# Kernel optimization log

Hardware: AMD Instinct MI355X
Metric: run time of the kernel (lower is better)

## Reference

```python
import jax, jax.numpy as jnp
import numpy as np

B, S, D = 1, 4096, 768
H = 12
HD = D // H  # 64


def setup_inputs() -> dict:
    key = jax.random.key(0)
    ks = jax.random.split(key, 6)
    sc = 1.0 / np.sqrt(D)
    return {
        "x": jax.random.normal(ks[0], (B, S, D), dtype=jnp.float32),
        "wq": jax.random.normal(ks[1], (D, D), dtype=jnp.float32) * sc,
        "wk": jax.random.normal(ks[2], (D, D), dtype=jnp.float32) * sc,
        "wv": jax.random.normal(ks[3], (D, D), dtype=jnp.float32) * sc,
        "wo": jax.random.normal(ks[4], (D, D), dtype=jnp.float32) * sc,
        "bo": jax.random.normal(ks[5], (D,), dtype=jnp.float32) * 0.02,
    }


def reference(x, wq, wk, wv, wo, bo):
    b, n, _ = x.shape
    # projections (torch Linear: x @ W.T; here weights stored as (d_in, d_out))
    q = (x @ wq).reshape(b, n, H, HD).transpose(0, 2, 1, 3)  # b h n d
    k = (x @ wk).reshape(b, n, H, HD).transpose(0, 2, 1, 3)
    v = (x @ wv).reshape(b, n, H, HD).transpose(0, 2, 1, 3)
    scores = jnp.einsum("bhqd,bhkd->bhqk", q, k)
    causal = jnp.tril(jnp.ones((n, n), dtype=bool))  # True = keep
    scores = jnp.where(causal, scores, -jnp.inf)
    weights = jax.nn.softmax(scores / np.sqrt(HD), axis=-1)
    ctx = jnp.einsum("bhqk,bhkd->bhqd", weights, v)
    ctx = ctx.transpose(0, 2, 1, 3).reshape(b, n, D)
    return ctx @ wo + bo
```

## Files before the change

kernel.cpp:

```cpp
#include <hip/hip_runtime.h>


typedef short bf16x8 __attribute__((ext_vector_type(8)));
typedef float f32x4 __attribute__((ext_vector_type(4)));
typedef unsigned short u16;

static constexpr int S_LEN = 4096;
static constexpr int DIM   = 768;
static constexpr int NH    = 12;
static constexpr float QSCALE = 0.125f * 1.44269504088896340736f;

__device__ inline u16 f2bf(float f) {
  union { float f; unsigned int u; } v; v.f = f;
  unsigned int r = v.u + 0x7FFFu + ((v.u >> 16) & 1u);
  return (u16)(r >> 16);
}

__device__ inline void gload_lds16(const u16* g, u16* s) {
  __builtin_amdgcn_global_load_lds(
      (const __attribute__((address_space(1))) unsigned int*)g,
      (__attribute__((address_space(3))) unsigned int*)s, 16, 0, 0);
}

__global__ __launch_bounds__(256)
void prep_kernel(const float* __restrict__ x, const float* __restrict__ w0,
                 const float* __restrict__ w1, const float* __restrict__ w2,
                 const float* __restrict__ w3, u16* __restrict__ xb,
                 u16* __restrict__ t0, u16* __restrict__ t1,
                 u16* __restrict__ t2, u16* __restrict__ t3) {
  if (blockIdx.z == 4) {
    const size_t n = (size_t)S_LEN * DIM;
    const int id = blockIdx.y * 12 + blockIdx.x;
    const size_t stride = (size_t)144 * 256 * 8;
    for (size_t i = ((size_t)id * 256 + threadIdx.x) * 8; i < n; i += stride) {
      const float4 a = *(const float4*)(x + i);
      const float4 b = *(const float4*)(x + i + 4);
      bf16x8 o;
      o[0] = (short)f2bf(a.x); o[1] = (short)f2bf(a.y);
      o[2] = (short)f2bf(a.z); o[3] = (short)f2bf(a.w);
      o[4] = (short)f2bf(b.x); o[5] = (short)f2bf(b.y);
      o[6] = (short)f2bf(b.z); o[7] = (short)f2bf(b.w);
      *(bf16x8*)(xb + i) = o;
    }
    return;
  }
  __shared__ float T[64][65];
  const float* src; u16* dst;
  switch (blockIdx.z) {
    case 0: src = w0; dst = t0; break;
    case 1: src = w1; dst = t1; break;
    case 2: src = w2; dst = t2; break;
    default: src = w3; dst = t3; break;
  }
  const int k0 = blockIdx.y * 64, n0 = blockIdx.x * 64;
  const int r = threadIdx.x >> 2, c0 = (threadIdx.x & 3) * 16;
#pragma unroll
  for (int i = 0; i < 4; ++i) {
    const float4 v = *(const float4*)(src + (size_t)(k0 + r) * DIM + n0 + c0 + i * 4);
    T[r][c0 + i * 4 + 0] = v.x;
    T[r][c0 + i * 4 + 1] = v.y;
    T[r][c0 + i * 4 + 2] = v.z;
    T[r][c0 + i * 4 + 3] = v.w;
  }
  __syncthreads();
  bf16x8 o0, o1;
#pragma unroll
  for (int i = 0; i < 8; ++i) {
    o0[i] = (short)f2bf(T[c0 + i][r]);
    o1[i] = (short)f2bf(T[c0 + 8 + i][r]);
  }
  *(bf16x8*)(dst + (size_t)(n0 + r) * DIM + k0 + c0) = o0;
  *(bf16x8*)(dst + (size_t)(n0 + r) * DIM + k0 + c0 + 8) = o1;
}

template <int MODE>
__global__ __launch_bounds__(256)
void mfma_gemm_kernel(const u16* __restrict__ A, const u16* __restrict__ Bq,
                      const u16* __restrict__ Bk, const u16* __restrict__ Bv,
                      const float* __restrict__ bias, u16* __restrict__ Qb,
                      u16* __restrict__ Kb, u16* __restrict__ VT,
                      float* __restrict__ Out) {
  constexpr int MT = (MODE == 0) ? 4 : 2;
  constexpr int BM = MT * 32;
  __shared__ __align__(16) u16 Al[BM * 64];
  __shared__ __align__(16) u16 Bl[96 * 64];

  const int tid  = threadIdx.x;
  const int wv   = tid >> 6;
  const int lane = tid & 63;
  const int quad = lane >> 4;
  const int l16  = lane & 15;
  const int wr = wv >> 1, wc = wv & 1;
  const int m0 = blockIdx.y * BM;
  const int n0 = blockIdx.x * 96;

  int wi = 0, nb = n0;
  const u16* BT = Bq;
  if (MODE == 0) {
    wi = n0 / DIM;
    nb = n0 - wi * DIM;
    BT = (wi == 0) ? Bq : (wi == 1) ? Bk : Bv;
  }

  const int sr8 = lane >> 3;
  const int sc  = ((lane & 7) ^ sr8) * 8;
  const int key = (l16 & 7);

  f32x4 acc[MT][3] = {};

  for (int k0 = 0; k0 < DIM; k0 += 64) {
    __syncthreads();
#pragma unroll
    for (int j = 0; j < MT; ++j)
      gload_lds16(A + (size_t)(m0 + wv * (BM / 4) + j * 8 + sr8) * DIM + k0 + sc,
                  &Al[(wv * (BM / 4) + j * 8) * 64]);
#pragma unroll
    for (int j = 0; j < 3; ++j)
      gload_lds16(BT + (size_t)(nb + wv * 24 + j * 8 + sr8) * DIM + k0 + sc,
                  &Bl[(wv * 24 + j * 8) * 64]);
    __syncthreads();

#pragma unroll
    for (int kh = 0; kh < 2; ++kh) {
      const int cb = kh * 4;
      bf16x8 af[MT], bfr[3];
#pragma unroll
      for (int mt = 0; mt < MT; ++mt) {
        const int row = wr * (BM / 2) + mt * 16 + l16;
        af[mt] = *(const bf16x8*)&Al[row * 64 + ((cb + quad) ^ key) * 8];
      }
#pragma unroll
      for (int nt = 0; nt < 3; ++nt) {
        const int row = wc * 48 + nt * 16 + l16;
        bfr[nt] = *(const bf16x8*)&Bl[row * 64 + ((cb + quad) ^ key) * 8];
      }
#pragma unroll
      for (int mt = 0; mt < MT; ++mt)
#pragma unroll
        for (int nt = 0; nt < 3; ++nt)
          acc[mt][nt] = __builtin_amdgcn_mfma_f32_16x16x32_bf16(
              af[mt], bfr[nt], acc[mt][nt], 0, 0, 0);
    }
  }

  const float sc_out = (MODE == 0 && wi == 0) ? QSCALE : 1.0f;
#pragma unroll
  for (int mt = 0; mt < MT; ++mt) {
#pragma unroll
    for (int nt = 0; nt < 3; ++nt) {
      const int row = m0 + wr * (BM / 2) + mt * 16 + quad * 4;
      const int nc  = wc * 48 + nt * 16 + l16;
      if (MODE == 0) {
        const int ncol = nb + nc;
        if (wi < 2) {
          u16* dst = (wi == 0) ? Qb : Kb;
#pragma unroll
          for (int r = 0; r < 4; ++r)
            dst[(size_t)(row + r) * DIM + ncol] = f2bf(acc[mt][nt][r] * sc_out);
        } else {
          u16 pk[4];
#pragma unroll
          for (int r = 0; r < 4; ++r) pk[r] = f2bf(acc[mt][nt][r]);
          unsigned long long v;
          __builtin_memcpy(&v, pk, 8);
          *(unsigned long long*)(VT + (size_t)ncol * S_LEN + row) = v;
        }
      } else {
        const int ncol = n0 + nc;
        const float bvv = bias[ncol];
#pragma unroll
        for (int r = 0; r < 4; ++r)
          Out[(size_t)(row + r) * DIM + ncol] = acc[mt][nt][r] + bvv;
      }
    }
  }
}

__global__ __launch_bounds__(256)
void attn_mfma_kernel(const u16* __restrict__ Qb, const u16* __restrict__ Kb,
                      const u16* __restrict__ VTb, u16* __restrict__ ctx) {
  __shared__ __align__(16) u16 Ql[32 * 72];
  __shared__ __align__(16) u16 Kl[128 * 64];
  __shared__ __align__(16) u16 Vl[64 * 128];
  __shared__ __align__(16) u16 Pl[4][16 * 72];
  __shared__ float4 lbuf[4][64];

  const int tid  = threadIdx.x;
  const int w    = tid >> 6;
  const int lane = tid & 63;
  const int quad = lane >> 4;
  const int l16  = lane & 15;
  const int qw   = w >> 1;
  const int kw   = w & 1;
  const int key  = l16 & 7;

  const int id = blockIdx.x;
  const int rc = id & 7, slot = id >> 3;
  const int h  = (slot < 64) ? rc : 8 + (rc >> 1);
  const int bx = (slot < 64) ? slot : ((rc & 1) * 32 + (slot - 64));

  const int sr8  = lane >> 3;
  const int scK  = ((lane & 7) ^ sr8) * 8;
  const int sr16 = lane >> 4;

#pragma unroll 1
  for (int side = 0; side < 2; ++side) {
    const int qt = side ? (127 - bx) : bx;
    const int q0 = qt * 32;

    __syncthreads();
    {
      const int row = tid >> 3, col = (tid & 7) * 8;
      *(bf16x8*)&Ql[row * 72 + col] =
          *(const bf16x8*)(Qb + (size_t)(q0 + row) * DIM + h * 64 + col);
    }

    f32x4 o[4] = {};
    float l_r[4] = {};

    const int nkt = qt / 2 + 1;
    const int niter = (nkt + 1) >> 1;
    const int my_last = nkt - 1;

#pragma unroll 1
    for (int i = 0; i < niter; ++i) {
      const int k0g = i * 128;
      __syncthreads();
#pragma unroll
      for (int j = 0; j < 4; ++j)
        gload_lds16(Kb + (size_t)(k0g + w * 32 + j * 8 + sr8) * DIM + h * 64 + scK,
                    &Kl[(w * 32 + j * 8) * 64]);
#pragma unroll
      for (int j = 0; j < 4; ++j) {
        const int vrow = w * 16 + j * 4 + sr16;
        const int vcol = ((lane & 15) ^ (vrow & 7)) * 8;
        gload_lds16(VTb + (size_t)(h * 64 + vrow) * S_LEN + k0g + vcol,
                    &Vl[(w * 16 + j * 4) * 128]);
      }
      __syncthreads();

      const int kt_w = 2 * i + kw;
      if (kt_w < nkt) {
        const bf16x8 aq0 = *(const bf16x8*)&Ql[(qw * 16 + l16) * 72 + quad * 8];
        const bf16x8 aq1 = *(const bf16x8*)&Ql[(qw * 16 + l16) * 72 + 32 + quad * 8];
        f32x4 s[4];
#pragma unroll
        for (int t = 0; t < 4; ++t) {
          const int row = kw * 64 + t * 16 + l16;
          const bf16x8 bk0 = *(const bf16x8*)&Kl[row * 64 + (quad ^ key) * 8];
          const bf16x8 bk1 = *(const bf16x8*)&Kl[row * 64 + ((quad ^ 4) ^ key) * 8];
          s[t] = __builtin_amdgcn_mfma_f32_16x16x32_bf16(aq0, bk0, f32x4{0.f,0.f,0.f,0.f}, 0, 0, 0);
          s[t] = __builtin_amdgcn_mfma_f32_16x16x32_bf16(aq1, bk1, s[t], 0, 0, 0);
        }

        if (kt_w == my_last) {
#pragma unroll
          for (int t = 0; t < 4; ++t)
#pragma unroll
            for (int r = 0; r < 4; ++r) {
              const int kvg = k0g + kw * 64 + t * 16 + l16;
              const int qg  = q0 + qw * 16 + quad * 4 + r;
              float p = __builtin_amdgcn_exp2f(s[t][r]);
              if (kvg > qg) p = 0.f;
              l_r[r] += p;
              Pl[w][(quad * 4 + r) * 72 + t * 16 + l16] =
                  (u16)((__float_as_uint(p) + 0x8000u) >> 16);
            }
        } else {
#pragma unroll
          for (int t = 0; t < 4; ++t)
#pragma unroll
            for (int r = 0; r < 4; ++r) {
              const float p = __builtin_amdgcn_exp2f(s[t][r]);
              l_r[r] += p;
              Pl[w][(quad * 4 + r) * 72 + t * 16 + l16] =
                  (u16)((__float_as_uint(p) + 0x8000u) >> 16);
            }
        }

        const bf16x8 pa0 = *(const bf16x8*)&Pl[w][l16 * 72 + quad * 8];
        const bf16x8 pa1 = *(const bf16x8*)&Pl[w][l16 * 72 + 32 + quad * 8];
#pragma unroll
        for (int t = 0; t < 4; ++t) {
          const int row = t * 16 + l16;
          const int c0 = (kw * 8 + quad) ^ key;
          const int c1 = (kw * 8 + quad + 4) ^ key;
          const bf16x8 vb0 = *(const bf16x8*)&Vl[row * 128 + c0 * 8];
          const bf16x8 vb1 = *(const bf16x8*)&Vl[row * 128 + c1 * 8];
          o[t] = __builtin_amdgcn_mfma_f32_16x16x32_bf16(pa0, vb0, o[t], 0, 0, 0);
          o[t] = __builtin_amdgcn_mfma_f32_16x16x32_bf16(pa1, vb1, o[t], 0, 0, 0);
        }
      }
    }

    __syncthreads();
    float* Obuf = (float*)Kl;
#pragma unroll
    for (int t = 0; t < 4; ++t)
      *(f32x4*)&Obuf[(w * 64 + lane) * 16 + t * 4] = o[t];
    lbuf[w][lane] = float4{l_r[0], l_r[1], l_r[2], l_r[3]};
    __syncthreads();
#pragma unroll
    for (int t = 0; t < 4; ++t) {
      const f32x4 po = *(const f32x4*)&Obuf[((w ^ 1) * 64 + lane) * 16 + t * 4];
      o[t] += po;
    }
    {
      const float4 pl = lbuf[w ^ 1][lane];
      l_r[0] += pl.x; l_r[1] += pl.y; l_r[2] += pl.z; l_r[3] += pl.w;
    }

    if (kw == 0) {
#pragma unroll
      for (int r = 0; r < 4; ++r) {
        float l = l_r[r];
        l += __shfl_xor(l, 1);
        l += __shfl_xor(l, 2);
        l += __shfl_xor(l, 4);
        l += __shfl_xor(l, 8);
        const float inv = 1.f / l;
        const int row = q0 + qw * 16 + quad * 4 + r;
#pragma unroll
        for (int t = 0; t < 4; ++t)
          ctx[(size_t)row * DIM + h * 64 + t * 16 + l16] = f2bf(o[t][r] * inv);
      }
    }
  }
}

extern "C" void kernel_launch(void* const* d_in, const int* in_sizes, int n_in,
                              void* d_out, int out_size, void* d_ws,
                              size_t ws_size, hipStream_t stream) {
  const float* x  = (const float*)d_in[0];
  const float* wq = (const float*)d_in[1];
  const float* wk = (const float*)d_in[2];
  const float* wv = (const float*)d_in[3];
  const float* wo = (const float*)d_in[4];
  const float* bo = (const float*)d_in[5];

  const size_t n_x = (size_t)S_LEN * DIM;
  const size_t n_w = (size_t)DIM * DIM;
  u16* xb  = (u16*)d_ws;
  u16* wtq = xb + n_x;
  u16* wtk = wtq + n_w;
  u16* wtv = wtk + n_w;
  u16* wto = wtv + n_w;
  u16* Qb  = wto + n_w;
  u16* Kb  = Qb + n_x;
  u16* VTb = Kb + n_x;
  u16* ctx = VTb + n_x;

  prep_kernel<<<dim3(12, 12, 5), 256, 0, stream>>>(
      x, wq, wk, wv, wo, xb, wtq, wtk, wtv, wto);

  mfma_gemm_kernel<0><<<dim3(24, 32), 256, 0, stream>>>(
      xb, wtq, wtk, wtv, nullptr, Qb, Kb, VTb, nullptr);

  attn_mfma_kernel<<<dim3(768), 256, 0, stream>>>(Qb, Kb, VTb, ctx);

  mfma_gemm_kernel<1><<<dim3(8, 64), 256, 0, stream>>>(
      ctx, wto, nullptr, nullptr, bo, nullptr, nullptr, nullptr, (float*)d_out);
}
```

Baseline: 183.0 us.

## Process both causal query tiles in one KV pass with double-buffered K/V

The attention kernel now loads both paired query tiles (front and mirrored back) at once, with each of four waves owning 16 query rows, and streams 64-key K/V tiles through a double-buffered LDS ring. The next tile is prefetched while the current one is computed. This drops the split-K-across-waves reduction through LDS and the second pass over K/V for the low tile, which lets the two tiles share K/V loads. In exchange, waves on the short tile go idle for much of the loop, so load balance across waves is worse, and there is only one barrier per iteration with async loads in flight.

```diff
diff --git a/kernel.cpp b/kernel.cpp
--- a/kernel.cpp
+++ b/kernel.cpp
@@ -179,19 +179,16 @@
 __global__ __launch_bounds__(256)
 void attn_mfma_kernel(const u16* __restrict__ Qb, const u16* __restrict__ Kb,
                       const u16* __restrict__ VTb, u16* __restrict__ ctx) {
-  __shared__ __align__(16) u16 Ql[32 * 72];
-  __shared__ __align__(16) u16 Kl[128 * 64];
-  __shared__ __align__(16) u16 Vl[64 * 128];
+  __shared__ __align__(16) u16 Ql[64 * 72];
+  __shared__ __align__(16) u16 Kl[2][64 * 64];
+  __shared__ __align__(16) u16 Vl[2][64 * 64];
   __shared__ __align__(16) u16 Pl[4][16 * 72];
-  __shared__ float4 lbuf[4][64];
 
   const int tid  = threadIdx.x;
   const int w    = tid >> 6;
   const int lane = tid & 63;
   const int quad = lane >> 4;
   const int l16  = lane & 15;
-  const int qw   = w >> 1;
-  const int kw   = w & 1;
   const int key  = l16 & 7;
 
   const int id = blockIdx.x;
@@ -199,132 +196,117 @@
   const int h  = (slot < 64) ? rc : 8 + (rc >> 1);
   const int bx = (slot < 64) ? slot : ((rc & 1) * 32 + (slot - 64));
 
-  const int sr8  = lane >> 3;
-  const int scK  = ((lane & 7) ^ sr8) * 8;
-  const int sr16 = lane >> 4;
+  const int q0A = bx * 32;
+  const int q0B = (127 - bx) * 32;
+  const int qlo = ((w < 2) ? q0A : q0B) + (w & 1) * 16;
+  const int nkt_w = ((qlo + 15) >> 6) + 1;
+  const int nktB  = ((q0B + 31) >> 6) + 1;
+
+  const int sr8 = lane >> 3;
+  const int sc  = ((lane & 7) ^ sr8) * 8;
+
+  {
+    const int qrow_s = tid >> 3;
+    const int qcol_s = (tid & 7) * 8;
+    *(bf16x8*)&Ql[qrow_s * 72 + qcol_s] =
+        *(const bf16x8*)(Qb + (size_t)(q0A + qrow_s) * DIM + h * 64 + qcol_s);
+    *(bf16x8*)&Ql[(32 + qrow_s) * 72 + qcol_s] =
+        *(const bf16x8*)(Qb + (size_t)(q0B + qrow_s) * DIM + h * 64 + qcol_s);
+  }
+#pragma unroll
+  for (int j = 0; j < 2; ++j) {
+    gload_lds16(Kb + (size_t)(w * 16 + j * 8 + sr8) * DIM + h * 64 + sc,
+                &Kl[0][(w * 16 + j * 8) * 64]);
+    gload_lds16(VTb + (size_t)(h * 64 + w * 16 + j * 8 + sr8) * S_LEN + sc,
+                &Vl[0][(w * 16 + j * 8) * 64]);
+  }
+  __syncthreads();
+
+  const bf16x8 aq0 = *(const bf16x8*)&Ql[(w * 16 + l16) * 72 + quad * 8];
+  const bf16x8 aq1 = *(const bf16x8*)&Ql[(w * 16 + l16) * 72 + 32 + quad * 8];
+
+  f32x4 o[4] = {};
+  float l_r[4] = {};
 
 #pragma unroll 1
-  for (int side = 0; side < 2; ++side) {
-    const int qt = side ? (127 - bx) : bx;
-    const int q0 = qt * 32;
-
+  for (int kt = 0; kt < nktB; ++kt) {
     __syncthreads();
-    {
-      const int row = tid >> 3, col = (tid & 7) * 8;
-      *(bf16x8*)&Ql[row * 72 + col] =
-          *(const bf16x8*)(Qb + (size_t)(q0 + row) * DIM + h * 64 + col);
-    }
-
-    f32x4 o[4] = {};
-    float l_r[4] = {};
-
-    const int nkt = qt / 2 + 1;
-    const int niter = (nkt + 1) >> 1;
-    const int my_last = nkt - 1;
-
-#pragma unroll 1
-    for (int i = 0; i < niter; ++i) {
-      const int k0g = i * 128;
-      __syncthreads();
-#pragma unroll
-      for (int j = 0; j < 4; ++j)
-        gload_lds16(Kb + (size_t)(k0g + w * 32 + j * 8 + sr8) * DIM + h * 64 + scK,
-                    &Kl[(w * 32 + j * 8) * 64]);
-#pragma unroll
-      for (int j = 0; j < 4; ++j) {
-        const int vrow = w * 16 + j * 4 + sr16;
-        const int vcol = ((lane & 15) ^ (vrow & 7)) * 8;
-        gload_lds16(VTb + (size_t)(h * 64 + vrow) * S_LEN + k0g + vcol,
-                    &Vl[(w * 16 + j * 4) * 128]);
-      }
-      __syncthreads();
-
-      const int kt_w = 2 * i + kw;
-      if (kt_w < nkt) {
-        const bf16x8 aq0 = *(const bf16x8*)&Ql[(qw * 16 + l16) * 72 + quad * 8];
-        const bf16x8 aq1 = *(const bf16x8*)&Ql[(qw * 16 + l16) * 72 + 32 + quad * 8];
-        f32x4 s[4];
-#pragma unroll
-        for (int t = 0; t < 4; ++t) {
-          const int row = kw * 64 + t * 16 + l16;
-          const bf16x8 bk0 = *(const bf16x8*)&Kl[row * 64 + (quad ^ key) * 8];
-          const bf16x8 bk1 = *(const bf16x8*)&Kl[row * 64 + ((quad ^ 4) ^ key) * 8];
-          s[t] = __builtin_amdgcn_mfma_f32_16x16x32_bf16(aq0, bk0, f32x4{0.f,0.f,0.f,0.f}, 0, 0, 0);
-          s[t] = __builtin_amdgcn_mfma_f32_16x16x32_bf16(aq1, bk1, s[t], 0, 0, 0);
-        }
-
-        if (kt_w == my_last) {
-#pragma unroll
-          for (int t = 0; t < 4; ++t)
-#pragma unroll
-            for (int r = 0; r < 4; ++r) {
-              const int kvg = k0g + kw * 64 + t * 16 + l16;
-              const int qg  = q0 + qw * 16 + quad * 4 + r;
-              float p = __builtin_amdgcn_exp2f(s[t][r]);
-              if (kvg > qg) p = 0.f;
-              l_r[r] += p;
-              Pl[w][(quad * 4 + r) * 72 + t * 16 + l16] =
-                  (u16)((__float_as_uint(p) + 0x8000u) >> 16);
-            }
-        } else {
-#pragma unroll
-          for (int t = 0; t < 4; ++t)
-#pragma unroll
-            for (int r = 0; r < 4; ++r) {
-              const float p = __builtin_amdgcn_exp2f(s[t][r]);
-              l_r[r] += p;
-              Pl[w][(quad * 4 + r) * 72 + t * 16 + l16] =
-                  (u16)((__float_as_uint(p) + 0x8000u) >> 16);
-            }
-        }
-
-        const bf16x8 pa0 = *(const bf16x8*)&Pl[w][l16 * 72 + quad * 8];
-        const bf16x8 pa1 = *(const bf16x8*)&Pl[w][l16 * 72 + 32 + quad * 8];
-#pragma unroll
-        for (int t = 0; t < 4; ++t) {
-          const int row = t * 16 + l16;
-          const int c0 = (kw * 8 + quad) ^ key;
-          const int c1 = (kw * 8 + quad + 4) ^ key;
-          const bf16x8 vb0 = *(const bf16x8*)&Vl[row * 128 + c0 * 8];
-          const bf16x8 vb1 = *(const bf16x8*)&Vl[row * 128 + c1 * 8];
-          o[t] = __builtin_amdgcn_mfma_f32_16x16x32_bf16(pa0, vb0, o[t], 0, 0, 0);
-          o[t] = __builtin_amdgcn_mfma_f32_16x16x32_bf16(pa1, vb1, o[t], 0, 0, 0);
-        }
-      }
-    }
-
-    __syncthreads();
-    float* Obuf = (float*)Kl;
+    const int b = kt & 1;
+
+    if (kt + 1 < nktB) {
+      const int kn = (kt + 1) * 64;
+#pragma unroll
+      for (int j = 0; j < 2; ++j) {
+        gload_lds16(Kb + (size_t)(kn + w * 16 + j * 8 + sr8) * DIM + h * 64 + sc,
+                    &Kl[b ^ 1][(w * 16 + j * 8) * 64]);
+        gload_lds16(VTb + (size_t)(h * 64 + w * 16 + j * 8 + sr8) * S_LEN + kn + sc,
+                    &Vl[b ^ 1][(w * 16 + j * 8) * 64]);
+      }
+    }
+
+    if (kt < nkt_w) {
+      const int k0 = kt * 64;
+      f32x4 s[4];
+#pragma unroll
+      for (int t = 0; t < 4; ++t) {
+        const int row = t * 16 + l16;
+        const bf16x8 bk0 = *(const bf16x8*)&Kl[b][row * 64 + (quad ^ key) * 8];
+        const bf16x8 bk1 = *(const bf16x8*)&Kl[b][row * 64 + ((quad ^ 4) ^ key) * 8];
+        s[t] = __builtin_amdgcn_mfma_f32_16x16x32_bf16(
+            aq0, bk0, f32x4{0.f, 0.f, 0.f, 0.f}, 0, 0, 0);
+        s[t] = __builtin_amdgcn_mfma_f32_16x16x32_bf16(aq1, bk1, s[t], 0, 0, 0);
+      }
+
+      if (kt == nkt_w - 1) {
+#pragma unroll
+        for (int t = 0; t < 4; ++t)
+#pragma unroll
+          for (int r = 0; r < 4; ++r) {
+            const int kvg = k0 + t * 16 + l16;
+            const int qg  = qlo + quad * 4 + r;
+            float p = __builtin_amdgcn_exp2f(s[t][r]);
+            if (kvg > qg) p = 0.f;
+            l_r[r] += p;
+            Pl[w][(quad * 4 + r) * 72 + t * 16 + l16] =
+                (u16)((__float_as_uint(p) + 0x8000u) >> 16);
+          }
+      } else {
+#pragma unroll
+        for (int t = 0; t < 4; ++t)
+#pragma unroll
+          for (int r = 0; r < 4; ++r) {
+            const float p = __builtin_amdgcn_exp2f(s[t][r]);
+            l_r[r] += p;
+            Pl[w][(quad * 4 + r) * 72 + t * 16 + l16] =
+                (u16)((__float_as_uint(p) + 0x8000u) >> 16);
+          }
+      }
+
+      const bf16x8 pa0 = *(const bf16x8*)&Pl[w][l16 * 72 + quad * 8];
+      const bf16x8 pa1 = *(const bf16x8*)&Pl[w][l16 * 72 + 32 + quad * 8];
+#pragma unroll
+      for (int t = 0; t < 4; ++t) {
+        const int row = t * 16 + l16;
+        const bf16x8 vb0 = *(const bf16x8*)&Vl[b][row * 64 + (quad ^ key) * 8];
+        const bf16x8 vb1 = *(const bf16x8*)&Vl[b][row * 64 + ((quad ^ 4) ^ key) * 8];
+        o[t] = __builtin_amdgcn_mfma_f32_16x16x32_bf16(pa0, vb0, o[t], 0, 0, 0);
+        o[t] = __builtin_amdgcn_mfma_f32_16x16x32_bf16(pa1, vb1, o[t], 0, 0, 0);
+      }
+    }
+  }
+
+#pragma unroll
+  for (int r = 0; r < 4; ++r) {
+    float l = l_r[r];
+    l += __shfl_xor(l, 1);
+    l += __shfl_xor(l, 2);
+    l += __shfl_xor(l, 4);
+    l += __shfl_xor(l, 8);
+    const float inv = 1.f / l;
+    const int row = qlo + quad * 4 + r;
 #pragma unroll
     for (int t = 0; t < 4; ++t)
-      *(f32x4*)&Obuf[(w * 64 + lane) * 16 + t * 4] = o[t];
-    lbuf[w][lane] = float4{l_r[0], l_r[1], l_r[2], l_r[3]};
-    __syncthreads();
-#pragma unroll
-    for (int t = 0; t < 4; ++t) {
-      const f32x4 po = *(const f32x4*)&Obuf[((w ^ 1) * 64 + lane) * 16 + t * 4];
-      o[t] += po;
-    }
-    {
-      const float4 pl = lbuf[w ^ 1][lane];
-      l_r[0] += pl.x; l_r[1] += pl.y; l_r[2] += pl.z; l_r[3] += pl.w;
-    }
-
-    if (kw == 0) {
-#pragma unroll
-      for (int r = 0; r < 4; ++r) {
-        float l = l_r[r];
-        l += __shfl_xor(l, 1);
-        l += __shfl_xor(l, 2);
-        l += __shfl_xor(l, 4);
-        l += __shfl_xor(l, 8);
-        const float inv = 1.f / l;
-        const int row = q0 + qw * 16 + quad * 4 + r;
-#pragma unroll
-        for (int t = 0; t < 4; ++t)
-          ctx[(size_t)row * DIM + h * 64 + t * 16 + l16] = f2bf(o[t][r] * inv);
-      }
-    }
+      ctx[(size_t)row * DIM + h * 64 + t * 16 + l16] = f2bf(o[t][r] * inv);
   }
 }
 
```

After: 193.5 us. 1.06x slower.
